# Optimization experiments

Measured on AMD Instinct MI355X. Metric: run time of the kernel, lower is better.

## Reference

```python
import jax, jax.numpy as jnp
import numpy as np

D = 256  # subgraph_width
N_CLASSES = 10
EPS = 1e-5  # torch LayerNorm default


def _layernorm(x, g, b):
    mu = jnp.mean(x, axis=-1, keepdims=True)
    var = jnp.var(x, axis=-1, keepdims=True)
    return (x - mu) * jax.lax.rsqrt(var + EPS) * g + b


def setup_inputs() -> dict:
    key = jax.random.key(0)
    ks = jax.random.split(key, 16)
    B, T, N = 64, 512, 512
    traj = jax.random.normal(ks[0], (B, T, 2), dtype=jnp.float32)
    labels = jax.random.randint(ks[1], (B,), 0, N_CLASSES)
    h = jax.random.normal(ks[2], (B, N, D), dtype=jnp.float32)
    valid_len = jnp.maximum(jax.random.randint(ks[3], (B,), 0, N), 1)
    s = 0.02
    params = dict(
        emb=jax.random.normal(ks[4], (N_CLASSES, D), dtype=jnp.float32) * s,
        w_mlp=jax.random.normal(ks[5], (2, D), dtype=jnp.float32) * s,
        b_mlp=jnp.zeros((D,), jnp.float32),
        ln_g=jnp.ones((D,), jnp.float32),
        ln_b=jnp.zeros((D,), jnp.float32),
        wq=jax.random.normal(ks[6], (D, D), dtype=jnp.float32) * s,
        bq=jnp.zeros((D,), jnp.float32),
        wk=jax.random.normal(ks[7], (D, D), dtype=jnp.float32) * s,
        bk=jnp.zeros((D,), jnp.float32),
        wv=jax.random.normal(ks[8], (D, D), dtype=jnp.float32) * s,
        bv=jnp.zeros((D,), jnp.float32),
        w_out=jax.random.normal(ks[9], (D, 1), dtype=jnp.float32) * s,
        b_out=jnp.zeros((1,), jnp.float32),
    )
    return dict(traj=traj, labels=labels, h=h, valid_len=valid_len, **params)


def reference(traj, labels, h, valid_len, emb, w_mlp, b_mlp, ln_g, ln_b,
              wq, bq, wk, bk, wv, bv, w_out, b_out):
    # MLP(in=2, out=D, activation='leaky'): Linear -> LayerNorm -> LeakyReLU
    x = jax.nn.leaky_relu(_layernorm(traj @ w_mlp + b_mlp, ln_g, ln_b))  # [B,T,D]
    le = emb[labels]                          # [B,D]
    x = x + le[:, None, :]                    # embed-add
    # SelfAttentionWithKeyFCLayer: Q from x, K/V from h, scaled, key-masked by valid_len
    q = x @ wq + bq                            # [B,T,D]
    k = h @ wk + bk                            # [B,N,D]
    v = h @ wv + bv                            # [B,N,D]
    scores = jnp.einsum('btd,bnd->btn', q, k) / jnp.sqrt(jnp.float32(D))
    N = h.shape[1]
    key_mask = jnp.arange(N)[None, :] < valid_len[:, None]          # [B,N]
    scores = jnp.where(key_mask[:, None, :], scores, jnp.float32(-1e9))
    attn = jax.nn.softmax(scores, axis=-1)
    enc = jnp.einsum('btn,bnd->btd', attn, v)  # [B,T,D]
    pooled = jnp.max(enc, axis=1) + le          # [B,D]
    return jax.nn.sigmoid(pooled @ w_out + b_out)  # [B,1]
```

## Files before the change

### kernel.cpp

```cpp
#include <hip/hip_runtime.h>
#include <math.h>

typedef float f32x4 __attribute__((ext_vector_type(4)));
typedef __bf16 bf16x8 __attribute__((ext_vector_type(8)));
typedef unsigned short u16x8 __attribute__((ext_vector_type(8)));
typedef unsigned short u16x4 __attribute__((ext_vector_type(4)));
typedef unsigned int u32x4 __attribute__((ext_vector_type(4)));

#define MFMA(a, b, c) __builtin_amdgcn_mfma_f32_16x16x32_bf16((a), (b), (c), 0, 0, 0)

static __device__ __forceinline__ unsigned short f2bf(float f) {
  unsigned u = __float_as_uint(f);
  u += 0x7FFFu + ((u >> 16) & 1u);
  return (unsigned short)(u >> 16);
}
static __device__ __forceinline__ float bf2f(unsigned short s) {
  return __uint_as_float(((unsigned)s) << 16);
}
static __device__ __forceinline__ unsigned pack2bf(float lo, float hi) {
  return (unsigned)f2bf(lo) | ((unsigned)f2bf(hi) << 16);
}

static __device__ __forceinline__ int swz512(int row, int col) {
  return row * 512 + (col ^ ((((row & 7) ^ (col >> 6)) & 7) << 4));
}
static __device__ __forceinline__ int swzV(int d, int col) {
  return d * 64 + (col ^ (((d >> 1) & 3) << 4));
}
static __device__ __forceinline__ int swzO(int d, int col) {
  return d * 256 + (col ^ ((((d & 7) ^ (col >> 7)) & 7) << 4));
}

__global__ __launch_bounds__(256) void setup(
    const float* __restrict__ w0m, const float* __restrict__ w1m, const float* __restrict__ w2m,
    unsigned short* __restrict__ t0m, unsigned short* __restrict__ t1m, unsigned short* __restrict__ t2m,
    const float* __restrict__ w_mlp, const float* __restrict__ b_mlp, float* __restrict__ lnsc,
    const int* __restrict__ vlen, int* __restrict__ tasktab) {
  int bid = blockIdx.x;
  int t = threadIdx.x;
  if (bid == 48) {
    float w0 = w_mlp[t], w1 = w_mlp[256 + t], bb = b_mlp[t];
    float v[9] = {w0, w1, bb, w0 * w0, w1 * w1, w0 * w1, w0 * bb, w1 * bb, bb * bb};
    __shared__ float red[4][9];
#pragma unroll
    for (int j = 0; j < 9; ++j) {
      float s = v[j];
#pragma unroll
      for (int off = 32; off >= 1; off >>= 1) s += __shfl_xor(s, off, 64);
      v[j] = s;
    }
    if ((t & 63) == 0)
      for (int j = 0; j < 9; ++j) red[t >> 6][j] = v[j];
    __syncthreads();
    if (t < 9) lnsc[t] = red[0][t] + red[1][t] + red[2][t] + red[3][t];
    return;
  }
  if (bid == 49) {
    __shared__ int srank[64];
    if (t < 64) {
      int vb = vlen[t], r = 0;
      for (int j = 0; j < 64; ++j) {
        int vj = vlen[j];
        r += (vj > vb) || (vj == vb && j < t);
      }
      srank[r] = t;
    }
    __syncthreads();
    if (t < 64) {
      int r = t, b = srank[r];
      int xcd = r & 7, a = r >> 3;
      for (int tt = 0; tt < 4; ++tt)
        tasktab[(a * 4 + tt) * 8 + xcd] = (b << 2) | tt;
    }
    return;
  }
  int m = bid >> 4, t16 = bid & 15;
  const float* w = (m == 0) ? w0m : (m == 1) ? w1m : w2m;
  unsigned short* o = (m == 0) ? t0m : (m == 1) ? t1m : t2m;
  __shared__ float sm[64][65];
  int bi = t16 >> 2, bj = t16 & 3;
  for (int kb = 0; kb < 16; ++kb) {
    int idx = kb * 256 + t;
    int r = idx >> 6, c = idx & 63;
    sm[r][c] = w[(bi * 64 + r) * 256 + bj * 64 + c];
  }
  __syncthreads();
  for (int kb = 0; kb < 16; ++kb) {
    int idx = kb * 256 + t;
    int r = idx >> 6, c = idx & 63;
    int d = bj * 64 + r, e = bi * 64 + c;
    o[(e >> 5) * 8192 + d * 32 + (e & 31)] = f2bf(sm[c][r]);
  }
}

static __device__ __forceinline__ void gemm_direct(
    const unsigned short* __restrict__ Bpk, const unsigned short* Alds,
    int w, int g, int c15, f32x4 (&acc)[4][4]) {
  const unsigned short* bp = Bpk + (w * 64 + c15) * 32 + 8 * g;
#pragma unroll
  for (int c = 0; c < 8; ++c) {
    bf16x8 bfv[4];
#pragma unroll
    for (int nt = 0; nt < 4; ++nt)
      bfv[nt] = *(const bf16x8*)(bp + c * 8192 + nt * 512);
    bf16x8 af[4];
#pragma unroll
    for (int at = 0; at < 4; ++at)
      af[at] = *(const bf16x8*)((char*)Alds + swz512(at * 16 + c15, c * 64 + 16 * g));
    __builtin_amdgcn_s_setprio(1);
#pragma unroll
    for (int at = 0; at < 4; ++at)
#pragma unroll
      for (int nt = 0; nt < 4; ++nt) acc[at][nt] = MFMA(af[at], bfv[nt], acc[at][nt]);
    __builtin_amdgcn_s_setprio(0);
  }
}

__global__ __launch_bounds__(256, 4) void gemms(
    const float* __restrict__ h, const int* __restrict__ vlen,
    const unsigned short* __restrict__ wkPk, const float* __restrict__ bk,
    const unsigned short* __restrict__ wvPk, const float* __restrict__ bv,
    unsigned short* __restrict__ kout, unsigned short* __restrict__ vT) {
  __shared__ unsigned short Alds[64 * 256];
  int tid = threadIdx.x, w = tid >> 6, lane = tid & 63, g = lane >> 4, c15 = lane & 15;
  int tile = blockIdx.x;
  int b = tile >> 3;
  int nbase = (tile & 7) * 64;
  if (nbase >= vlen[b]) return;
  f32x4 acc[4][4];
  {
    const float* hb = h + (size_t)tile * 16384;
    f32x4 ha[8], hc[8];
#pragma unroll
    for (int i = 0; i < 8; ++i) {
      ha[i] = *(const f32x4*)(hb + i * 2048 + tid * 8);
      hc[i] = *(const f32x4*)(hb + i * 2048 + tid * 8 + 4);
    }
#pragma unroll
    for (int i = 0; i < 8; ++i) {
      u16x8 pk;
#pragma unroll
      for (int j = 0; j < 4; ++j) { pk[j] = f2bf(ha[i][j]); pk[j + 4] = f2bf(hc[i][j]); }
      *(u16x8*)((char*)Alds + swz512(i * 8 + (tid >> 5), (tid & 31) * 16)) = pk;
    }
  }
#pragma unroll
  for (int a = 0; a < 4; ++a)
#pragma unroll
    for (int n = 0; n < 4; ++n) acc[a][n] = (f32x4){0.f, 0.f, 0.f, 0.f};
  __syncthreads();

  gemm_direct(wvPk, Alds, w, g, c15, acc);
#pragma unroll
  for (int at = 0; at < 4; ++at)
#pragma unroll
    for (int nt = 0; nt < 4; ++nt) {
      int col = w * 64 + nt * 16 + c15;
      float bb = bv[col];
      u16x4 o;
#pragma unroll
      for (int r = 0; r < 4; ++r) o[r] = f2bf(acc[at][nt][r] + bb);
      *(u16x4*)(vT + (size_t)b * 131072 + (size_t)col * 512 + nbase + at * 16 + 4 * g) = o;
    }

#pragma unroll
  for (int a = 0; a < 4; ++a)
#pragma unroll
    for (int n = 0; n < 4; ++n) acc[a][n] = (f32x4){0.f, 0.f, 0.f, 0.f};
  gemm_direct(wkPk, Alds, w, g, c15, acc);
  __syncthreads();
#pragma unroll
  for (int at = 0; at < 4; ++at)
#pragma unroll
    for (int nt = 0; nt < 4; ++nt) {
      int col = w * 64 + nt * 16 + c15;
      float bb = bk[col];
#pragma unroll
      for (int r = 0; r < 4; ++r)
        *(unsigned short*)((char*)Alds + swz512(at * 16 + 4 * g + r, col * 2)) =
            f2bf(acc[at][nt][r] + bb);
    }
  __syncthreads();
  {
    int row = tid >> 2;
    for (int i = 0; i < 8; ++i) {
      int colb = (tid & 3) * 128 + i * 16;
      u16x8 vv = *(const u16x8*)((char*)Alds + swz512(row, colb));
      *(u16x8*)(kout + (size_t)(tile * 64 + row) * 256 + colb / 2) = vv;
    }
  }
}

__global__ __launch_bounds__(512, 2) void attn(
    const float* __restrict__ traj, const int* __restrict__ labels,
    const float* __restrict__ emb, const float* __restrict__ w_mlp,
    const float* __restrict__ b_mlp, const float* __restrict__ ln_g,
    const float* __restrict__ ln_b, const float* __restrict__ lnsc,
    const unsigned short* __restrict__ wqPk, const float* __restrict__ bq,
    const unsigned short* __restrict__ k, const unsigned short* __restrict__ vT,
    const int* __restrict__ valid_len, const int* __restrict__ tasktab,
    float* __restrict__ partial) {
  __shared__ unsigned short buf[2][16384];

  int task = tasktab[blockIdx.x];
  int b = task >> 2, tt = task & 3;
  int tid = threadIdx.x, w = tid >> 6, lane = tid & 63, g = lane >> 4, c15 = lane & 15;
  int vl = valid_len[b];
  int nit = (vl + 31) >> 5;
  bool isA = (w < 4);
  int wq4 = w & 3;

  {
    int rrow = tid >> 5, cb = (tid & 31) * 8;
    int lab = labels[b];
    f32x4 wa0 = *(const f32x4*)(w_mlp + cb), wa1 = *(const f32x4*)(w_mlp + cb + 4);
    f32x4 wb0 = *(const f32x4*)(w_mlp + 256 + cb), wb1 = *(const f32x4*)(w_mlp + 256 + cb + 4);
    f32x4 bm0 = *(const f32x4*)(b_mlp + cb), bm1 = *(const f32x4*)(b_mlp + cb + 4);
    f32x4 g0 = *(const f32x4*)(ln_g + cb), g1 = *(const f32x4*)(ln_g + cb + 4);
    f32x4 lb0 = *(const f32x4*)(ln_b + cb), lb1 = *(const f32x4*)(ln_b + cb + 4);
    f32x4 le0 = *(const f32x4*)(emb + lab * 256 + cb), le1 = *(const f32x4*)(emb + lab * 256 + cb + 4);
    float s0 = lnsc[0], s1 = lnsc[1], s2 = lnsc[2], s3 = lnsc[3], s4 = lnsc[4],
          s5 = lnsc[5], s6 = lnsc[6], s7 = lnsc[7], s8 = lnsc[8];
#pragma unroll
    for (int i = 0; i < 8; ++i) {
      int row = i * 16 + rrow, grow = b * 512 + tt * 128 + row;
      float t0 = traj[grow * 2], t1 = traj[grow * 2 + 1];
      float mu = (t0 * s0 + t1 * s1 + s2) * (1.f / 256.f);
      float ea2 = (t0 * t0 * s3 + t1 * t1 * s4 + s8 +
                   2.f * (t0 * t1 * s5 + t0 * s6 + t1 * s7)) * (1.f / 256.f);
      float rstd = rsqrtf(ea2 - mu * mu + 1e-5f);
      u16x8 pk;
#pragma unroll
      for (int j = 0; j < 4; ++j) {
        float a0 = t0 * wa0[j] + t1 * wb0[j] + bm0[j];
        float y0 = (a0 - mu) * rstd * g0[j] + lb0[j];
        pk[j] = f2bf((y0 > 0.f ? y0 : 0.01f * y0) + le0[j]);
        float a1 = t0 * wa1[j] + t1 * wb1[j] + bm1[j];
        float y1 = (a1 - mu) * rstd * g1[j] + lb1[j];
        pk[j + 4] = f2bf((y1 > 0.f ? y1 : 0.01f * y1) + le1[j]);
      }
      *(u16x8*)((char*)buf + swz512(row, cb * 2)) = pk;
    }
  }
  __syncthreads();

  {
    f32x4 qacc[4][4];
#pragma unroll
    for (int a = 0; a < 4; ++a)
#pragma unroll
      for (int n = 0; n < 4; ++n) qacc[a][n] = (f32x4){0.f, 0.f, 0.f, 0.f};
    int rbase = (w >> 2) * 64;
    const unsigned short* bp = wqPk + (wq4 * 64 + c15) * 32 + 8 * g;
#pragma unroll
    for (int c = 0; c < 8; ++c) {
      bf16x8 bfv[4];
#pragma unroll
      for (int nt = 0; nt < 4; ++nt)
        bfv[nt] = *(const bf16x8*)(bp + c * 8192 + nt * 512);
      bf16x8 af[4];
#pragma unroll
      for (int at = 0; at < 4; ++at)
        af[at] = *(const bf16x8*)((char*)buf + swz512(rbase + at * 16 + c15, c * 64 + 16 * g));
      __builtin_amdgcn_s_setprio(1);
#pragma unroll
      for (int at = 0; at < 4; ++at)
#pragma unroll
        for (int nt = 0; nt < 4; ++nt) qacc[at][nt] = MFMA(af[at], bfv[nt], qacc[at][nt]);
      __builtin_amdgcn_s_setprio(0);
    }
    __syncthreads();
#pragma unroll
    for (int nt = 0; nt < 4; ++nt) {
      int col = wq4 * 64 + nt * 16 + c15;
      float bb = bq[col];
#pragma unroll
      for (int at = 0; at < 4; ++at)
#pragma unroll
        for (int r = 0; r < 4; ++r)
          *(unsigned short*)((char*)buf + swz512(rbase + at * 16 + 4 * g + r, col * 2)) =
              f2bf(qacc[at][nt][r] + bb);
    }
  }
  __syncthreads();
  bf16x8 qf[2][8];
  if (isA) {
#pragma unroll
    for (int qt = 0; qt < 2; ++qt)
#pragma unroll
      for (int kk = 0; kk < 8; ++kk)
        qf[qt][kk] = *(const bf16x8*)((char*)buf + swz512(qt * 64 + wq4 * 16 + c15, kk * 64 + 16 * g));
  }
  __syncthreads();

  f32x4 acco[2][16];
#pragma unroll
  for (int qt = 0; qt < 2; ++qt)
#pragma unroll
    for (int i = 0; i < 16; ++i) acco[qt][i] = (f32x4){0.f, 0.f, 0.f, 0.f};
  float rs[2] = {0.f, 0.f};

  const unsigned short* kbase = k + (size_t)b * 512 * 256;
  const unsigned short* vbase = vT + (size_t)b * 131072;
  int t2 = tid & 255;

  if (!isA) {
    u16x8 kp[4], vp[4];
#pragma unroll
    for (int i = 0; i < 4; ++i) {
      int idx = t2 + 256 * i, key = idx >> 5, s = idx & 31;
      kp[i] = *(const u16x8*)(kbase + (size_t)key * 256 + s * 8);
    }
#pragma unroll
    for (int i = 0; i < 4; ++i) {
      int idx = t2 + 256 * i, d = idx >> 2, s = idx & 3;
      vp[i] = *(const u16x8*)(vbase + (size_t)d * 512 + s * 8);
    }
#pragma unroll
    for (int i = 0; i < 4; ++i) {
      int idx = t2 + 256 * i, key = idx >> 5, s = idx & 31;
      *(u16x8*)((char*)buf[0] + swz512(key, s * 16)) = kp[i];
    }
#pragma unroll
    for (int i = 0; i < 4; ++i) {
      int idx = t2 + 256 * i, d = idx >> 2, s = idx & 3;
      *(u16x8*)((char*)(buf[0] + 8192) + swzV(d, s * 16)) = vp[i];
    }
  }

  for (int it = 0; it < nit; ++it) {
    __syncthreads();
    if (isA) {
      const unsigned short* Klds = buf[it & 1];
      const unsigned short* Vlds = buf[it & 1] + 8192;
      int n0 = it * 32;
      f32x4 s4[2][2];
#pragma unroll
      for (int qt = 0; qt < 2; ++qt)
#pragma unroll
        for (int c = 0; c < 2; ++c) s4[qt][c] = (f32x4){0.f, 0.f, 0.f, 0.f};
      __builtin_amdgcn_s_setprio(1);
#pragma unroll
      for (int c = 0; c < 2; ++c)
#pragma unroll
        for (int kk = 0; kk < 8; ++kk) {
          bf16x8 kf = *(const bf16x8*)((char*)Klds + swz512(c * 16 + c15, kk * 64 + 16 * g));
          s4[0][c] = MFMA(kf, qf[0][kk], s4[0][c]);
          s4[1][c] = MFMA(kf, qf[1][kk], s4[1][c]);
        }
      __builtin_amdgcn_s_setprio(0);
      unsigned u01[2][2], u23[2][2];
#pragma unroll
      for (int qt = 0; qt < 2; ++qt)
#pragma unroll
        for (int c = 0; c < 2; ++c) {
          float p4[4];
#pragma unroll
          for (int r = 0; r < 4; ++r) {
            int key = n0 + c * 16 + 4 * g + r;
            float pv = (key < vl) ? __expf(s4[qt][c][r] * 0.0625f) : 0.f;
            p4[r] = pv;
            rs[qt] += pv;
          }
          u01[qt][c] = pack2bf(p4[0], p4[1]);
          u23[qt][c] = pack2bf(p4[2], p4[3]);
        }
      int srcA = c15 | ((lane & 16) << 1);
      int srcB = srcA + 16;
      bool hi = g >= 2;
      union { u32x4 u; bf16x8 v; } pa[2];
#pragma unroll
      for (int qt = 0; qt < 2; ++qt) {
        unsigned x0a = (unsigned)__shfl((int)u01[qt][0], srcA, 64);
        unsigned x1a = (unsigned)__shfl((int)u01[qt][1], srcA, 64);
        unsigned x0b = (unsigned)__shfl((int)u23[qt][0], srcA, 64);
        unsigned x1b = (unsigned)__shfl((int)u23[qt][1], srcA, 64);
        unsigned x0c = (unsigned)__shfl((int)u01[qt][0], srcB, 64);
        unsigned x1c = (unsigned)__shfl((int)u01[qt][1], srcB, 64);
        unsigned x0d = (unsigned)__shfl((int)u23[qt][0], srcB, 64);
        unsigned x1d = (unsigned)__shfl((int)u23[qt][1], srcB, 64);
        pa[qt].u[0] = hi ? x1a : x0a;
        pa[qt].u[1] = hi ? x1b : x0b;
        pa[qt].u[2] = hi ? x1c : x0c;
        pa[qt].u[3] = hi ? x1d : x0d;
      }
      __builtin_amdgcn_s_setprio(1);
#pragma unroll
      for (int dt = 0; dt < 16; ++dt) {
        bf16x8 vf = *(const bf16x8*)((char*)Vlds + swzV(dt * 16 + c15, 16 * g));
        acco[0][dt] = MFMA(vf, pa[0].v, acco[0][dt]);
        acco[1][dt] = MFMA(vf, pa[1].v, acco[1][dt]);
      }
      __builtin_amdgcn_s_setprio(0);
    } else if (it + 1 < nit) {
      int n1 = (it + 1) * 32;
      unsigned short* Kn = buf[(it + 1) & 1];
      unsigned short* Vn = buf[(it + 1) & 1] + 8192;
      u16x8 kp[4], vp[4];
#pragma unroll
      for (int i = 0; i < 4; ++i) {
        int idx = t2 + 256 * i, key = idx >> 5, s = idx & 31;
        kp[i] = *(const u16x8*)(kbase + (size_t)(n1 + key) * 256 + s * 8);
      }
#pragma unroll
      for (int i = 0; i < 4; ++i) {
        int idx = t2 + 256 * i, d = idx >> 2, s = idx & 3;
        vp[i] = *(const u16x8*)(vbase + (size_t)d * 512 + n1 + s * 8);
      }
#pragma unroll
      for (int i = 0; i < 4; ++i) {
        int idx = t2 + 256 * i, key = idx >> 5, s = idx & 31;
        *(u16x8*)((char*)Kn + swz512(key, s * 16)) = kp[i];
      }
#pragma unroll
      for (int i = 0; i < 4; ++i) {
        int idx = t2 + 256 * i, d = idx >> 2, s = idx & 3;
        *(u16x8*)((char*)Vn + swzV(d, s * 16)) = vp[i];
      }
    }
  }

  float inv[2];
  if (isA) {
#pragma unroll
    for (int qt = 0; qt < 2; ++qt) {
      rs[qt] += __shfl_xor(rs[qt], 16, 64);
      rs[qt] += __shfl_xor(rs[qt], 32, 64);
      inv[qt] = 1.f / rs[qt];
    }
  }
  __syncthreads();
  if (isA) {
#pragma unroll
    for (int qt = 0; qt < 2; ++qt) {
      int qcol = qt * 64 + wq4 * 16 + c15;
#pragma unroll
      for (int dt = 0; dt < 16; ++dt)
#pragma unroll
        for (int r = 0; r < 4; ++r) {
          int d = dt * 16 + 4 * g + r;
          *(unsigned short*)((char*)buf + swzO(d, qcol * 2)) = f2bf(acco[qt][dt][r] * inv[qt]);
        }
    }
  }
  __syncthreads();
  {
    int d = tid & 255, half = tid >> 8;
    float m = -1e30f;
    for (int i = 0; i < 8; ++i) {
      u16x8 vv = *(const u16x8*)((char*)buf + swzO(d, half * 128 + i * 16));
#pragma unroll
      for (int j = 0; j < 8; ++j) m = fmaxf(m, bf2f(vv[j]));
    }
    partial[(((size_t)b * 4 + tt) * 2 + half) * 256 + d] = m;
  }
}

__global__ __launch_bounds__(256) void finalize(
    const float* __restrict__ partial, const float* __restrict__ emb,
    const int* __restrict__ labels, const float* __restrict__ w_out,
    const float* __restrict__ b_out, float* __restrict__ out) {
  int b = blockIdx.x, t = threadIdx.x;
  float m = -1e30f;
#pragma unroll
  for (int s8 = 0; s8 < 8; ++s8)
    m = fmaxf(m, partial[((size_t)b * 8 + s8) * 256 + t]);
  m += emb[labels[b] * 256 + t];
  __shared__ float red[256];
  red[t] = m * w_out[t];
  __syncthreads();
  for (int s = 128; s > 0; s >>= 1) {
    if (t < s) red[t] += red[t + s];
    __syncthreads();
  }
  if (t == 0) out[b] = 1.f / (1.f + __expf(-(red[0] + b_out[0])));
}

extern "C" void kernel_launch(void* const* d_in, const int* in_sizes, int n_in,
                              void* d_out, int out_size, void* d_ws, size_t ws_size,
                              hipStream_t stream) {
  const float* traj   = (const float*)d_in[0];
  const int*   labels = (const int*)d_in[1];
  const float* h      = (const float*)d_in[2];
  const int*   vlen   = (const int*)d_in[3];
  const float* emb    = (const float*)d_in[4];
  const float* w_mlp  = (const float*)d_in[5];
  const float* b_mlp  = (const float*)d_in[6];
  const float* ln_g   = (const float*)d_in[7];
  const float* ln_b   = (const float*)d_in[8];
  const float* wq     = (const float*)d_in[9];
  const float* bq     = (const float*)d_in[10];
  const float* wk     = (const float*)d_in[11];
  const float* bk     = (const float*)d_in[12];
  const float* wv     = (const float*)d_in[13];
  const float* bv     = (const float*)d_in[14];
  const float* w_out  = (const float*)d_in[15];
  const float* b_out  = (const float*)d_in[16];
  float* out = (float*)d_out;

  unsigned short* kb   = (unsigned short*)d_ws;
  unsigned short* vT   = kb + (size_t)32768 * 256;
  unsigned short* wqPk = vT + (size_t)32768 * 256;
  unsigned short* wkPk = wqPk + 65536;
  unsigned short* wvPk = wkPk + 65536;
  float* lnsc    = (float*)(wvPk + 65536);
  float* partial = lnsc + 16;
  int*   tasktab = (int*)(partial + 64 * 8 * 256);

  setup<<<50, 256, 0, stream>>>(wq, wk, wv, wqPk, wkPk, wvPk, w_mlp, b_mlp, lnsc,
                                vlen, tasktab);
  gemms<<<512, 256, 0, stream>>>(h, vlen, wkPk, bk, wvPk, bv, kb, vT);
  attn<<<256, 512, 0, stream>>>(traj, labels, emb, w_mlp, b_mlp, ln_g, ln_b, lnsc,
                                wqPk, bq, kb, vT, vlen, tasktab, partial);
  finalize<<<64, 256, 0, stream>>>(partial, emb, labels, w_out, b_out, out);
}
```

Measured before the change: 79.06 us.

## Split key range across all eight waves and read K/V fragments directly from global

Replaces the producer/consumer split (four waves staging K/V into LDS, four computing) with all eight waves computing attention on alternating 32-key chunks. K and V fragments are loaded straight from global memory into MFMA operands, removing the LDS staging and the per-iteration block barrier. The two halves' partial outputs and row sums are then combined through LDS before normalisation. This doubles the compute waves but relies on cache hits for uncoalesced global fragment loads, and adds a reduction step.

```diff
diff --git a/kernel.cpp b/kernel.cpp
--- a/kernel.cpp
+++ b/kernel.cpp
@@ -23,9 +23,6 @@
 
 static __device__ __forceinline__ int swz512(int row, int col) {
   return row * 512 + (col ^ ((((row & 7) ^ (col >> 6)) & 7) << 4));
-}
-static __device__ __forceinline__ int swzV(int d, int col) {
-  return d * 64 + (col ^ (((d >> 1) & 3) << 4));
 }
 static __device__ __forceinline__ int swzO(int d, int col) {
   return d * 256 + (col ^ ((((d & 7) ^ (col >> 7)) & 7) << 4));
@@ -201,14 +198,15 @@
     const int* __restrict__ valid_len, const int* __restrict__ tasktab,
     float* __restrict__ partial) {
   __shared__ unsigned short buf[2][16384];
+  __shared__ float rsbuf[2][4][64];
 
   int task = tasktab[blockIdx.x];
   int b = task >> 2, tt = task & 3;
   int tid = threadIdx.x, w = tid >> 6, lane = tid & 63, g = lane >> 4, c15 = lane & 15;
   int vl = valid_len[b];
   int nit = (vl + 31) >> 5;
-  bool isA = (w < 4);
-  int wq4 = w & 3;
+  int qg = w & 3;
+  int ph = w >> 2;
 
   {
     int rrow = tid >> 5, cb = (tid & 31) * 8;
@@ -250,8 +248,8 @@
     for (int a = 0; a < 4; ++a)
 #pragma unroll
       for (int n = 0; n < 4; ++n) qacc[a][n] = (f32x4){0.f, 0.f, 0.f, 0.f};
-    int rbase = (w >> 2) * 64;
-    const unsigned short* bp = wqPk + (wq4 * 64 + c15) * 32 + 8 * g;
+    int rbase = ph * 64;
+    const unsigned short* bp = wqPk + (qg * 64 + c15) * 32 + 8 * g;
 #pragma unroll
     for (int c = 0; c < 8; ++c) {
       bf16x8 bfv[4];
@@ -272,7 +270,7 @@
     __syncthreads();
 #pragma unroll
     for (int nt = 0; nt < 4; ++nt) {
-      int col = wq4 * 64 + nt * 16 + c15;
+      int col = qg * 64 + nt * 16 + c15;
       float bb = bq[col];
 #pragma unroll
       for (int at = 0; at < 4; ++at)
@@ -284,13 +282,11 @@
   }
   __syncthreads();
   bf16x8 qf[2][8];
-  if (isA) {
-#pragma unroll
-    for (int qt = 0; qt < 2; ++qt)
-#pragma unroll
-      for (int kk = 0; kk < 8; ++kk)
-        qf[qt][kk] = *(const bf16x8*)((char*)buf + swz512(qt * 64 + wq4 * 16 + c15, kk * 64 + 16 * g));
-  }
+#pragma unroll
+  for (int qt = 0; qt < 2; ++qt)
+#pragma unroll
+    for (int kk = 0; kk < 8; ++kk)
+      qf[qt][kk] = *(const bf16x8*)((char*)buf + swz512(qt * 64 + qg * 16 + c15, kk * 64 + 16 * g));
   __syncthreads();
 
   f32x4 acco[2][16];
@@ -302,138 +298,122 @@
 
   const unsigned short* kbase = k + (size_t)b * 512 * 256;
   const unsigned short* vbase = vT + (size_t)b * 131072;
-  int t2 = tid & 255;
-
-  if (!isA) {
-    u16x8 kp[4], vp[4];
-#pragma unroll
-    for (int i = 0; i < 4; ++i) {
-      int idx = t2 + 256 * i, key = idx >> 5, s = idx & 31;
-      kp[i] = *(const u16x8*)(kbase + (size_t)key * 256 + s * 8);
-    }
-#pragma unroll
-    for (int i = 0; i < 4; ++i) {
-      int idx = t2 + 256 * i, d = idx >> 2, s = idx & 3;
-      vp[i] = *(const u16x8*)(vbase + (size_t)d * 512 + s * 8);
-    }
-#pragma unroll
-    for (int i = 0; i < 4; ++i) {
-      int idx = t2 + 256 * i, key = idx >> 5, s = idx & 31;
-      *(u16x8*)((char*)buf[0] + swz512(key, s * 16)) = kp[i];
-    }
-#pragma unroll
-    for (int i = 0; i < 4; ++i) {
-      int idx = t2 + 256 * i, d = idx >> 2, s = idx & 3;
-      *(u16x8*)((char*)(buf[0] + 8192) + swzV(d, s * 16)) = vp[i];
-    }
-  }
-
-  for (int it = 0; it < nit; ++it) {
-    __syncthreads();
-    if (isA) {
-      const unsigned short* Klds = buf[it & 1];
-      const unsigned short* Vlds = buf[it & 1] + 8192;
-      int n0 = it * 32;
-      f32x4 s4[2][2];
-#pragma unroll
-      for (int qt = 0; qt < 2; ++qt)
-#pragma unroll
-        for (int c = 0; c < 2; ++c) s4[qt][c] = (f32x4){0.f, 0.f, 0.f, 0.f};
-      __builtin_amdgcn_s_setprio(1);
-#pragma unroll
-      for (int c = 0; c < 2; ++c)
-#pragma unroll
-        for (int kk = 0; kk < 8; ++kk) {
-          bf16x8 kf = *(const bf16x8*)((char*)Klds + swz512(c * 16 + c15, kk * 64 + 16 * g));
-          s4[0][c] = MFMA(kf, qf[0][kk], s4[0][c]);
-          s4[1][c] = MFMA(kf, qf[1][kk], s4[1][c]);
+  const unsigned short* kx = kbase + (size_t)c15 * 256 + 8 * g;
+  const unsigned short* vx = vbase + (size_t)c15 * 512 + 8 * g;
+
+  for (int it = ph; it < nit; it += 2) {
+    int n0 = it * 32;
+    f32x4 s4[2][2];
+#pragma unroll
+    for (int qt = 0; qt < 2; ++qt)
+#pragma unroll
+      for (int c = 0; c < 2; ++c) s4[qt][c] = (f32x4){0.f, 0.f, 0.f, 0.f};
+    __builtin_amdgcn_s_setprio(1);
+#pragma unroll
+    for (int c = 0; c < 2; ++c)
+#pragma unroll
+      for (int kk = 0; kk < 8; ++kk) {
+        bf16x8 kf = *(const bf16x8*)(kx + (n0 + c * 16) * 256 + kk * 32);
+        s4[0][c] = MFMA(kf, qf[0][kk], s4[0][c]);
+        s4[1][c] = MFMA(kf, qf[1][kk], s4[1][c]);
+      }
+    __builtin_amdgcn_s_setprio(0);
+    unsigned u01[2][2], u23[2][2];
+#pragma unroll
+    for (int qt = 0; qt < 2; ++qt)
+#pragma unroll
+      for (int c = 0; c < 2; ++c) {
+        float p4[4];
+#pragma unroll
+        for (int r = 0; r < 4; ++r) {
+          int key = n0 + c * 16 + 4 * g + r;
+          float pv = (key < vl) ? __expf(s4[qt][c][r] * 0.0625f) : 0.f;
+          p4[r] = pv;
+          rs[qt] += pv;
         }
-      __builtin_amdgcn_s_setprio(0);
-      unsigned u01[2][2], u23[2][2];
-#pragma unroll
-      for (int qt = 0; qt < 2; ++qt)
-#pragma unroll
-        for (int c = 0; c < 2; ++c) {
-          float p4[4];
-#pragma unroll
-          for (int r = 0; r < 4; ++r) {
-            int key = n0 + c * 16 + 4 * g + r;
-            float pv = (key < vl) ? __expf(s4[qt][c][r] * 0.0625f) : 0.f;
-            p4[r] = pv;
-            rs[qt] += pv;
-          }
-          u01[qt][c] = pack2bf(p4[0], p4[1]);
-          u23[qt][c] = pack2bf(p4[2], p4[3]);
-        }
-      int srcA = c15 | ((lane & 16) << 1);
-      int srcB = srcA + 16;
-      bool hi = g >= 2;
-      union { u32x4 u; bf16x8 v; } pa[2];
-#pragma unroll
-      for (int qt = 0; qt < 2; ++qt) {
-        unsigned x0a = (unsigned)__shfl((int)u01[qt][0], srcA, 64);
-        unsigned x1a = (unsigned)__shfl((int)u01[qt][1], srcA, 64);
-        unsigned x0b = (unsigned)__shfl((int)u23[qt][0], srcA, 64);
-        unsigned x1b = (unsigned)__shfl((int)u23[qt][1], srcA, 64);
-        unsigned x0c = (unsigned)__shfl((int)u01[qt][0], srcB, 64);
-        unsigned x1c = (unsigned)__shfl((int)u01[qt][1], srcB, 64);
-        unsigned x0d = (unsigned)__shfl((int)u23[qt][0], srcB, 64);
-        unsigned x1d = (unsigned)__shfl((int)u23[qt][1], srcB, 64);
-        pa[qt].u[0] = hi ? x1a : x0a;
-        pa[qt].u[1] = hi ? x1b : x0b;
-        pa[qt].u[2] = hi ? x1c : x0c;
-        pa[qt].u[3] = hi ? x1d : x0d;
+        u01[qt][c] = pack2bf(p4[0], p4[1]);
+        u23[qt][c] = pack2bf(p4[2], p4[3]);
       }
-      __builtin_amdgcn_s_setprio(1);
-#pragma unroll
-      for (int dt = 0; dt < 16; ++dt) {
-        bf16x8 vf = *(const bf16x8*)((char*)Vlds + swzV(dt * 16 + c15, 16 * g));
-        acco[0][dt] = MFMA(vf, pa[0].v, acco[0][dt]);
-        acco[1][dt] = MFMA(vf, pa[1].v, acco[1][dt]);
-      }
-      __builtin_amdgcn_s_setprio(0);
-    } else if (it + 1 < nit) {
-      int n1 = (it + 1) * 32;
-      unsigned short* Kn = buf[(it + 1) & 1];
-      unsigned short* Vn = buf[(it + 1) & 1] + 8192;
-      u16x8 kp[4], vp[4];
-#pragma unroll
-      for (int i = 0; i < 4; ++i) {
-        int idx = t2 + 256 * i, key = idx >> 5, s = idx & 31;
-        kp[i] = *(const u16x8*)(kbase + (size_t)(n1 + key) * 256 + s * 8);
-      }
-#pragma unroll
-      for (int i = 0; i < 4; ++i) {
-        int idx = t2 + 256 * i, d = idx >> 2, s = idx & 3;
-        vp[i] = *(const u16x8*)(vbase + (size_t)d * 512 + n1 + s * 8);
-      }
-#pragma unroll
-      for (int i = 0; i < 4; ++i) {
-        int idx = t2 + 256 * i, key = idx >> 5, s = idx & 31;
-        *(u16x8*)((char*)Kn + swz512(key, s * 16)) = kp[i];
-      }
-#pragma unroll
-      for (int i = 0; i < 4; ++i) {
-        int idx = t2 + 256 * i, d = idx >> 2, s = idx & 3;
-        *(u16x8*)((char*)Vn + swzV(d, s * 16)) = vp[i];
-      }
-    }
-  }
-
+    int srcA = c15 | ((lane & 16) << 1);
+    int srcB = srcA + 16;
+    bool hi = g >= 2;
+    union { u32x4 u; bf16x8 v; } pa[2];
+#pragma unroll
+    for (int qt = 0; qt < 2; ++qt) {
+      unsigned x0a = (unsigned)__shfl((int)u01[qt][0], srcA, 64);
+      unsigned x1a = (unsigned)__shfl((int)u01[qt][1], srcA, 64);
+      unsigned x0b = (unsigned)__shfl((int)u23[qt][0], srcA, 64);
+      unsigned x1b = (unsigned)__shfl((int)u23[qt][1], srcA, 64);
+      unsigned x0c = (unsigned)__shfl((int)u01[qt][0], srcB, 64);
+      unsigned x1c = (unsigned)__shfl((int)u01[qt][1], srcB, 64);
+      unsigned x0d = (unsigned)__shfl((int)u23[qt][0], srcB, 64);
+      unsigned x1d = (unsigned)__shfl((int)u23[qt][1], srcB, 64);
+      pa[qt].u[0] = hi ? x1a : x0a;
+      pa[qt].u[1] = hi ? x1b : x0b;
+      pa[qt].u[2] = hi ? x1c : x0c;
+      pa[qt].u[3] = hi ? x1d : x0d;
+    }
+    __builtin_amdgcn_s_setprio(1);
+#pragma unroll
+    for (int dt = 0; dt < 16; ++dt) {
+      bf16x8 vf = *(const bf16x8*)(vx + dt * 8192 + n0);
+      acco[0][dt] = MFMA(vf, pa[0].v, acco[0][dt]);
+      acco[1][dt] = MFMA(vf, pa[1].v, acco[1][dt]);
+    }
+    __builtin_amdgcn_s_setprio(0);
+  }
+
+#pragma unroll
+  for (int qt = 0; qt < 2; ++qt) {
+    rs[qt] += __shfl_xor(rs[qt], 16, 64);
+    rs[qt] += __shfl_xor(rs[qt], 32, 64);
+  }
+
+  float* cbuf = (float*)buf;
+  if (ph == 1) {
+#pragma unroll
+    for (int dt = 0; dt < 16; ++dt)
+#pragma unroll
+      for (int r = 0; r < 4; ++r)
+        cbuf[(qg * 64 + dt * 4 + r) * 64 + lane] = acco[0][dt][r];
+    rsbuf[0][qg][lane] = rs[0];
+    rsbuf[1][qg][lane] = rs[1];
+  }
+  __syncthreads();
+  if (ph == 0) {
+#pragma unroll
+    for (int dt = 0; dt < 16; ++dt)
+#pragma unroll
+      for (int r = 0; r < 4; ++r)
+        acco[0][dt][r] += cbuf[(qg * 64 + dt * 4 + r) * 64 + lane];
+    rs[0] += rsbuf[0][qg][lane];
+    rs[1] += rsbuf[1][qg][lane];
+  }
+  __syncthreads();
+  if (ph == 1) {
+#pragma unroll
+    for (int dt = 0; dt < 16; ++dt)
+#pragma unroll
+      for (int r = 0; r < 4; ++r)
+        cbuf[(qg * 64 + dt * 4 + r) * 64 + lane] = acco[1][dt][r];
+  }
+  __syncthreads();
   float inv[2];
-  if (isA) {
+  if (ph == 0) {
+#pragma unroll
+    for (int dt = 0; dt < 16; ++dt)
+#pragma unroll
+      for (int r = 0; r < 4; ++r)
+        acco[1][dt][r] += cbuf[(qg * 64 + dt * 4 + r) * 64 + lane];
+    inv[0] = 1.f / rs[0];
+    inv[1] = 1.f / rs[1];
+  }
+  __syncthreads();
+
+  if (ph == 0) {
 #pragma unroll
     for (int qt = 0; qt < 2; ++qt) {
-      rs[qt] += __shfl_xor(rs[qt], 16, 64);
-      rs[qt] += __shfl_xor(rs[qt], 32, 64);
-      inv[qt] = 1.f / rs[qt];
-    }
-  }
-  __syncthreads();
-  if (isA) {
-#pragma unroll
-    for (int qt = 0; qt < 2; ++qt) {
-      int qcol = qt * 64 + wq4 * 16 + c15;
+      int qcol = qt * 64 + qg * 16 + c15;
 #pragma unroll
       for (int dt = 0; dt < 16; ++dt)
 #pragma unroll
```

New measurement: 112.1 us. +41.8%, slower.

## Software-pipeline attention loop with triple-buffered K/V ring and packed bf16 convert

Applied to the files above, without the earlier changes.

The K/V double buffer becomes a three-slot LDS ring so producer waves prefetch two tiles ahead. Compute waves now run QK^T and softmax for the next tile before PV for the current one, so score MFMAs overlap the exp and shuffle work. The manual bf16 rounding pack is replaced by the v_cvt_pk_bf16_f32 instruction. LDS use grows from 64KB to 96KB per block, which may break the two-blocks-per-CU occupancy target set by the launch bounds.

```diff
diff --git a/kernel.cpp b/kernel.cpp
--- a/kernel.cpp
+++ b/kernel.cpp
@@ -17,8 +17,10 @@
 static __device__ __forceinline__ float bf2f(unsigned short s) {
   return __uint_as_float(((unsigned)s) << 16);
 }
-static __device__ __forceinline__ unsigned pack2bf(float lo, float hi) {
-  return (unsigned)f2bf(lo) | ((unsigned)f2bf(hi) << 16);
+static __device__ __forceinline__ unsigned cvt_pk(float lo, float hi) {
+  unsigned r;
+  asm("v_cvt_pk_bf16_f32 %0, %1, %2" : "=v"(r) : "v"(lo), "v"(hi));
+  return r;
 }
 
 static __device__ __forceinline__ int swz512(int row, int col) {
@@ -200,7 +202,7 @@
     const unsigned short* __restrict__ k, const unsigned short* __restrict__ vT,
     const int* __restrict__ valid_len, const int* __restrict__ tasktab,
     float* __restrict__ partial) {
-  __shared__ unsigned short buf[2][16384];
+  __shared__ unsigned short ring[3][16384];
 
   int task = tasktab[blockIdx.x];
   int b = task >> 2, tt = task & 3;
@@ -219,14 +221,14 @@
     f32x4 g0 = *(const f32x4*)(ln_g + cb), g1 = *(const f32x4*)(ln_g + cb + 4);
     f32x4 lb0 = *(const f32x4*)(ln_b + cb), lb1 = *(const f32x4*)(ln_b + cb + 4);
     f32x4 le0 = *(const f32x4*)(emb + lab * 256 + cb), le1 = *(const f32x4*)(emb + lab * 256 + cb + 4);
-    float s0 = lnsc[0], s1 = lnsc[1], s2 = lnsc[2], s3 = lnsc[3], s4 = lnsc[4],
+    float s0 = lnsc[0], s1 = lnsc[1], s2 = lnsc[2], s3 = lnsc[3], s4_ = lnsc[4],
           s5 = lnsc[5], s6 = lnsc[6], s7 = lnsc[7], s8 = lnsc[8];
 #pragma unroll
     for (int i = 0; i < 8; ++i) {
       int row = i * 16 + rrow, grow = b * 512 + tt * 128 + row;
       float t0 = traj[grow * 2], t1 = traj[grow * 2 + 1];
       float mu = (t0 * s0 + t1 * s1 + s2) * (1.f / 256.f);
-      float ea2 = (t0 * t0 * s3 + t1 * t1 * s4 + s8 +
+      float ea2 = (t0 * t0 * s3 + t1 * t1 * s4_ + s8 +
                    2.f * (t0 * t1 * s5 + t0 * s6 + t1 * s7)) * (1.f / 256.f);
       float rstd = rsqrtf(ea2 - mu * mu + 1e-5f);
       u16x8 pk;
@@ -239,7 +241,7 @@
         float y1 = (a1 - mu) * rstd * g1[j] + lb1[j];
         pk[j + 4] = f2bf((y1 > 0.f ? y1 : 0.01f * y1) + le1[j]);
       }
-      *(u16x8*)((char*)buf + swz512(row, cb * 2)) = pk;
+      *(u16x8*)((char*)ring + swz512(row, cb * 2)) = pk;
     }
   }
   __syncthreads();
@@ -261,7 +263,7 @@
       bf16x8 af[4];
 #pragma unroll
       for (int at = 0; at < 4; ++at)
-        af[at] = *(const bf16x8*)((char*)buf + swz512(rbase + at * 16 + c15, c * 64 + 16 * g));
+        af[at] = *(const bf16x8*)((char*)ring + swz512(rbase + at * 16 + c15, c * 64 + 16 * g));
       __builtin_amdgcn_s_setprio(1);
 #pragma unroll
       for (int at = 0; at < 4; ++at)
@@ -278,7 +280,7 @@
       for (int at = 0; at < 4; ++at)
 #pragma unroll
         for (int r = 0; r < 4; ++r)
-          *(unsigned short*)((char*)buf + swz512(rbase + at * 16 + 4 * g + r, col * 2)) =
+          *(unsigned short*)((char*)ring + swz512(rbase + at * 16 + 4 * g + r, col * 2)) =
               f2bf(qacc[at][nt][r] + bb);
     }
   }
@@ -289,7 +291,7 @@
     for (int qt = 0; qt < 2; ++qt)
 #pragma unroll
       for (int kk = 0; kk < 8; ++kk)
-        qf[qt][kk] = *(const bf16x8*)((char*)buf + swz512(qt * 64 + wq4 * 16 + c15, kk * 64 + 16 * g));
+        qf[qt][kk] = *(const bf16x8*)((char*)ring + swz512(qt * 64 + wq4 * 16 + c15, kk * 64 + 16 * g));
   }
   __syncthreads();
 
@@ -299,125 +301,123 @@
 #pragma unroll
     for (int i = 0; i < 16; ++i) acco[qt][i] = (f32x4){0.f, 0.f, 0.f, 0.f};
   float rs[2] = {0.f, 0.f};
+  f32x4 s4[2][2];
+  union Pa { u32x4 u; bf16x8 v; };
+  Pa paC[2], paN[2];
 
   const unsigned short* kbase = k + (size_t)b * 512 * 256;
   const unsigned short* vbase = vT + (size_t)b * 131072;
   int t2 = tid & 255;
 
-  if (!isA) {
+  auto STAGE = [&](int slot, int n0) {
     u16x8 kp[4], vp[4];
 #pragma unroll
     for (int i = 0; i < 4; ++i) {
       int idx = t2 + 256 * i, key = idx >> 5, s = idx & 31;
-      kp[i] = *(const u16x8*)(kbase + (size_t)key * 256 + s * 8);
+      kp[i] = *(const u16x8*)(kbase + (size_t)(n0 + key) * 256 + s * 8);
     }
 #pragma unroll
     for (int i = 0; i < 4; ++i) {
       int idx = t2 + 256 * i, d = idx >> 2, s = idx & 3;
-      vp[i] = *(const u16x8*)(vbase + (size_t)d * 512 + s * 8);
+      vp[i] = *(const u16x8*)(vbase + (size_t)d * 512 + n0 + s * 8);
     }
 #pragma unroll
     for (int i = 0; i < 4; ++i) {
       int idx = t2 + 256 * i, key = idx >> 5, s = idx & 31;
-      *(u16x8*)((char*)buf[0] + swz512(key, s * 16)) = kp[i];
+      *(u16x8*)((char*)ring[slot] + swz512(key, s * 16)) = kp[i];
     }
 #pragma unroll
     for (int i = 0; i < 4; ++i) {
       int idx = t2 + 256 * i, d = idx >> 2, s = idx & 3;
-      *(u16x8*)((char*)(buf[0] + 8192) + swzV(d, s * 16)) = vp[i];
-    }
-  }
+      *(u16x8*)((char*)(ring[slot] + 8192) + swzV(d, s * 16)) = vp[i];
+    }
+  };
+
+  auto QKT = [&](int slot) {
+#pragma unroll
+    for (int qt = 0; qt < 2; ++qt)
+#pragma unroll
+      for (int c = 0; c < 2; ++c) s4[qt][c] = (f32x4){0.f, 0.f, 0.f, 0.f};
+    __builtin_amdgcn_s_setprio(1);
+#pragma unroll
+    for (int c = 0; c < 2; ++c)
+#pragma unroll
+      for (int kk = 0; kk < 8; ++kk) {
+        bf16x8 kf = *(const bf16x8*)((char*)ring[slot] + swz512(c * 16 + c15, kk * 64 + 16 * g));
+        s4[0][c] = MFMA(kf, qf[0][kk], s4[0][c]);
+        s4[1][c] = MFMA(kf, qf[1][kk], s4[1][c]);
+      }
+    __builtin_amdgcn_s_setprio(0);
+  };
+
+  auto SOFTMAX = [&](int n0, Pa (&po)[2]) {
+    unsigned u01[2][2], u23[2][2];
+#pragma unroll
+    for (int qt = 0; qt < 2; ++qt)
+#pragma unroll
+      for (int c = 0; c < 2; ++c) {
+        float p4[4];
+#pragma unroll
+        for (int r = 0; r < 4; ++r) {
+          int key = n0 + c * 16 + 4 * g + r;
+          float pv = (key < vl) ? __expf(s4[qt][c][r] * 0.0625f) : 0.f;
+          p4[r] = pv;
+          rs[qt] += pv;
+        }
+        u01[qt][c] = cvt_pk(p4[0], p4[1]);
+        u23[qt][c] = cvt_pk(p4[2], p4[3]);
+      }
+    int srcA = c15 | ((lane & 16) << 1);
+    int srcB = srcA + 16;
+    bool hi = g >= 2;
+#pragma unroll
+    for (int qt = 0; qt < 2; ++qt) {
+      unsigned x0a = (unsigned)__shfl((int)u01[qt][0], srcA, 64);
+      unsigned x1a = (unsigned)__shfl((int)u01[qt][1], srcA, 64);
+      unsigned x0b = (unsigned)__shfl((int)u23[qt][0], srcA, 64);
+      unsigned x1b = (unsigned)__shfl((int)u23[qt][1], srcA, 64);
+      unsigned x0c = (unsigned)__shfl((int)u01[qt][0], srcB, 64);
+      unsigned x1c = (unsigned)__shfl((int)u01[qt][1], srcB, 64);
+      unsigned x0d = (unsigned)__shfl((int)u23[qt][0], srcB, 64);
+      unsigned x1d = (unsigned)__shfl((int)u23[qt][1], srcB, 64);
+      po[qt].u[0] = hi ? x1a : x0a;
+      po[qt].u[1] = hi ? x1b : x0b;
+      po[qt].u[2] = hi ? x1c : x0c;
+      po[qt].u[3] = hi ? x1d : x0d;
+    }
+  };
+
+  auto PV = [&](int slot) {
+    const unsigned short* Vlds = ring[slot] + 8192;
+    __builtin_amdgcn_s_setprio(1);
+#pragma unroll
+    for (int dt = 0; dt < 16; ++dt) {
+      bf16x8 vf = *(const bf16x8*)((char*)Vlds + swzV(dt * 16 + c15, 16 * g));
+      acco[0][dt] = MFMA(vf, paC[0].v, acco[0][dt]);
+      acco[1][dt] = MFMA(vf, paC[1].v, acco[1][dt]);
+    }
+    __builtin_amdgcn_s_setprio(0);
+  };
+
+  if (!isA) STAGE(0, 0);
+  __syncthreads();
+  if (isA) QKT(0);
+  if (!isA && 1 < nit) STAGE(1, 32);
+  if (isA) SOFTMAX(0, paC);
+  __syncthreads();
 
   for (int it = 0; it < nit; ++it) {
+    if (isA) {
+      if (it + 1 < nit) {
+        QKT((it + 1) % 3);
+        SOFTMAX((it + 1) * 32, paN);
+      }
+      PV(it % 3);
+      if (it + 1 < nit) { paC[0] = paN[0]; paC[1] = paN[1]; }
+    } else if (it + 2 < nit) {
+      STAGE((it + 2) % 3, (it + 2) * 32);
+    }
     __syncthreads();
-    if (isA) {
-      const unsigned short* Klds = buf[it & 1];
-      const unsigned short* Vlds = buf[it & 1] + 8192;
-      int n0 = it * 32;
-      f32x4 s4[2][2];
-#pragma unroll
-      for (int qt = 0; qt < 2; ++qt)
-#pragma unroll
-        for (int c = 0; c < 2; ++c) s4[qt][c] = (f32x4){0.f, 0.f, 0.f, 0.f};
-      __builtin_amdgcn_s_setprio(1);
-#pragma unroll
-      for (int c = 0; c < 2; ++c)
-#pragma unroll
-        for (int kk = 0; kk < 8; ++kk) {
-          bf16x8 kf = *(const bf16x8*)((char*)Klds + swz512(c * 16 + c15, kk * 64 + 16 * g));
-          s4[0][c] = MFMA(kf, qf[0][kk], s4[0][c]);
-          s4[1][c] = MFMA(kf, qf[1][kk], s4[1][c]);
-        }
-      __builtin_amdgcn_s_setprio(0);
-      unsigned u01[2][2], u23[2][2];
-#pragma unroll
-      for (int qt = 0; qt < 2; ++qt)
-#pragma unroll
-        for (int c = 0; c < 2; ++c) {
-          float p4[4];
-#pragma unroll
-          for (int r = 0; r < 4; ++r) {
-            int key = n0 + c * 16 + 4 * g + r;
-            float pv = (key < vl) ? __expf(s4[qt][c][r] * 0.0625f) : 0.f;
-            p4[r] = pv;
-            rs[qt] += pv;
-          }
-          u01[qt][c] = pack2bf(p4[0], p4[1]);
-          u23[qt][c] = pack2bf(p4[2], p4[3]);
-        }
-      int srcA = c15 | ((lane & 16) << 1);
-      int srcB = srcA + 16;
-      bool hi = g >= 2;
-      union { u32x4 u; bf16x8 v; } pa[2];
-#pragma unroll
-      for (int qt = 0; qt < 2; ++qt) {
-        unsigned x0a = (unsigned)__shfl((int)u01[qt][0], srcA, 64);
-        unsigned x1a = (unsigned)__shfl((int)u01[qt][1], srcA, 64);
-        unsigned x0b = (unsigned)__shfl((int)u23[qt][0], srcA, 64);
-        unsigned x1b = (unsigned)__shfl((int)u23[qt][1], srcA, 64);
-        unsigned x0c = (unsigned)__shfl((int)u01[qt][0], srcB, 64);
-        unsigned x1c = (unsigned)__shfl((int)u01[qt][1], srcB, 64);
-        unsigned x0d = (unsigned)__shfl((int)u23[qt][0], srcB, 64);
-        unsigned x1d = (unsigned)__shfl((int)u23[qt][1], srcB, 64);
-        pa[qt].u[0] = hi ? x1a : x0a;
-        pa[qt].u[1] = hi ? x1b : x0b;
-        pa[qt].u[2] = hi ? x1c : x0c;
-        pa[qt].u[3] = hi ? x1d : x0d;
-      }
-      __builtin_amdgcn_s_setprio(1);
-#pragma unroll
-      for (int dt = 0; dt < 16; ++dt) {
-        bf16x8 vf = *(const bf16x8*)((char*)Vlds + swzV(dt * 16 + c15, 16 * g));
-        acco[0][dt] = MFMA(vf, pa[0].v, acco[0][dt]);
-        acco[1][dt] = MFMA(vf, pa[1].v, acco[1][dt]);
-      }
-      __builtin_amdgcn_s_setprio(0);
-    } else if (it + 1 < nit) {
-      int n1 = (it + 1) * 32;
-      unsigned short* Kn = buf[(it + 1) & 1];
-      unsigned short* Vn = buf[(it + 1) & 1] + 8192;
-      u16x8 kp[4], vp[4];
-#pragma unroll
-      for (int i = 0; i < 4; ++i) {
-        int idx = t2 + 256 * i, key = idx >> 5, s = idx & 31;
-        kp[i] = *(const u16x8*)(kbase + (size_t)(n1 + key) * 256 + s * 8);
-      }
-#pragma unroll
-      for (int i = 0; i < 4; ++i) {
-        int idx = t2 + 256 * i, d = idx >> 2, s = idx & 3;
-        vp[i] = *(const u16x8*)(vbase + (size_t)d * 512 + n1 + s * 8);
-      }
-#pragma unroll
-      for (int i = 0; i < 4; ++i) {
-        int idx = t2 + 256 * i, key = idx >> 5, s = idx & 31;
-        *(u16x8*)((char*)Kn + swz512(key, s * 16)) = kp[i];
-      }
-#pragma unroll
-      for (int i = 0; i < 4; ++i) {
-        int idx = t2 + 256 * i, d = idx >> 2, s = idx & 3;
-        *(u16x8*)((char*)Vn + swzV(d, s * 16)) = vp[i];
-      }
-    }
   }
 
   float inv[2];
@@ -439,7 +439,7 @@
 #pragma unroll
         for (int r = 0; r < 4; ++r) {
           int d = dt * 16 + 4 * g + r;
-          *(unsigned short*)((char*)buf + swzO(d, qcol * 2)) = f2bf(acco[qt][dt][r] * inv[qt]);
+          *(unsigned short*)((char*)ring + swzO(d, qcol * 2)) = f2bf(acco[qt][dt][r] * inv[qt]);
         }
     }
   }
@@ -448,7 +448,7 @@
     int d = tid & 255, half = tid >> 8;
     float m = -1e30f;
     for (int i = 0; i < 8; ++i) {
-      u16x8 vv = *(const u16x8*)((char*)buf + swzO(d, half * 128 + i * 16));
+      u16x8 vv = *(const u16x8*)((char*)ring + swzO(d, half * 128 + i * 16));
 #pragma unroll
       for (int j = 0; j < 8; ++j) m = fmaxf(m, bf2f(vv[j]));
     }
```

New measurement: 118.3 us. 49.6% more time.
